# Optimization experiments

Measured on AMD Instinct MI355X. Metric: run time of the kernel, lower is better.

The kernel has to match this reference:

```python
import jax, jax.numpy as jnp
import numpy as np

HEADS = 8
DIM = 512
SCALE = (DIM // HEADS) ** (-0.5)  # 0.125


def setup_inputs() -> dict:
    key = jax.random.key(0)
    k1, k2, k3, k4 = jax.random.split(key, 4)
    B, C, H, W = 4, DIM, 96, 96
    x = jax.random.normal(k1, (B, C, H, W), dtype=jnp.float32)
    # 1x1 conv weights collapsed to matrices [out_ch, in_ch]
    w_qkv = jax.random.normal(k2, (3 * DIM, DIM), dtype=jnp.float32) * (DIM ** -0.5)
    w_out = jax.random.normal(k3, (DIM, DIM), dtype=jnp.float32) * (DIM ** -0.5)
    b_out = jax.random.normal(k4, (DIM,), dtype=jnp.float32) * 0.01
    return {"x": x, "w_qkv": w_qkv, "w_out": w_out, "b_out": b_out}


def reference(x, w_qkv, w_out, b_out):
    # axis='height' branch of the original forward
    b, c, h, w = x.shape
    heads = HEADS
    d = c // heads
    # 1x1 conv == per-pixel GEMM: [B,3C,H,W]
    qkv = jnp.einsum('bchw,oc->bohw', x, w_qkv)
    # 'b (qkv heads d) x y -> qkv b heads x y d'
    qkv = qkv.reshape(b, 3, heads, d, h, w)
    qkv = jnp.transpose(qkv, (1, 0, 2, 4, 5, 3))  # [3, b, heads, h, w, d]
    q, k, v = qkv[0], qkv[1], qkv[2]
    # attention along the width axis, batched over (b, heads, row x)
    dots = jnp.einsum('bhxid,bhxjd->bhxij', q, k) * SCALE
    attn = jax.nn.softmax(dots, axis=-1)
    out = jnp.einsum('bhxij,bhxjd->bhxid', attn, v)  # [b, heads, h, w, d]
    # 'b heads x y d -> b (heads d) x y'
    out = jnp.transpose(out, (0, 1, 4, 2, 3)).reshape(b, heads * d, h, w)
    # to_out 1x1 conv with bias
    out = jnp.einsum('bchw,oc->bohw', out, w_out) + b_out[None, :, None, None]
    return out
```

## Files before the change

### kernel.cpp

```cpp
#include <hip/hip_runtime.h>

typedef unsigned short u16;
typedef unsigned int u32;
typedef __attribute__((ext_vector_type(8))) short short8;
typedef __attribute__((ext_vector_type(4))) float floatx4;

#define HEADS 8
#define DIM 512
#define HH 96
#define WW 96
#define NPIX 9216
#define M_TOT 36864
#define N_QKV 1536
#define SCALE 0.125f

__device__ __forceinline__ float b2f(u16 v){
    union{float f;u32 u;}x; x.u=((u32)v)<<16; return x.f;
}
__device__ __forceinline__ u16 f2b(float f){
    union{float f;u32 u;}x; x.f=f;
    u32 u=x.u + 0x7fffu + ((x.u>>16)&1u);
    return (u16)(u>>16);
}
__device__ __forceinline__ u32 pack2(float a,float b){
    return (u32)f2b(a) | ((u32)f2b(b)<<16);
}

__device__ __forceinline__ void gload16(const u16* g, u16* l){
    __builtin_amdgcn_global_load_lds(
        (const __attribute__((address_space(1))) u32*)g,
        (__attribute__((address_space(3))) u32*)l, 16, 0, 0);
}

__global__ void detect_dtype(const u16* __restrict__ wq, int* __restrict__ flag){
    __shared__ int cnt;
    if (threadIdx.x==0) cnt=0;
    __syncthreads();
    u16 u = wq[2*threadIdx.x];
    int e = (u>>7)&0xff;
    if (e>=100 && e<=128) atomicAdd(&cnt,1);
    __syncthreads();
    if (threadIdx.x==0) *flag = (cnt>128)?1:0;
}

__global__ __launch_bounds__(256)
void convert_w(const void* __restrict__ wq, const void* __restrict__ wo,
               const int* __restrict__ flag, u16* __restrict__ wqb, u16* __restrict__ wob){
    const int isb = *flag;
    int i = blockIdx.x*256 + threadIdx.x;
    const int nq = N_QKV*DIM;
    if (i < nq){
        wqb[i] = isb ? ((const u16*)wq)[i] : f2b(((const float*)wq)[i]);
    } else {
        int j = i - nq;
        wob[j] = isb ? ((const u16*)wo)[j] : f2b(((const float*)wo)[j]);
    }
}

__global__ __launch_bounds__(256)
void convert_x(const void* __restrict__ xv, const int* __restrict__ flag,
               u16* __restrict__ xb){
    __shared__ u16 tile[64][65];
    const int isb = *flag;
    const int p0 = blockIdx.x*64, c0 = blockIdx.y*64, b = blockIdx.z;
    const int t = threadIdx.x;
    const int pl = t&63, c4 = t>>6;
    const float* x32 = (const float*)xv;
    const u16*   x16 = (const u16*)xv;
    size_t src = ((size_t)b*DIM + c0 + c4)*NPIX + p0 + pl;
    #pragma unroll
    for (int i=0;i<16;i++){
        int cl = c4 + i*4;
        size_t s = src + (size_t)i*4*NPIX;
        tile[cl][pl] = isb ? x16[s] : f2b(x32[s]);
    }
    __syncthreads();
    const int cu = t&31, r8 = t>>5;
    u32* xb32 = (u32*)xb;
    #pragma unroll
    for (int i=0;i<8;i++){
        int pr = r8 + i*8;
        u32 v = (u32)tile[2*cu][pr] | ((u32)tile[2*cu+1][pr]<<16);
        xb32[((size_t)b*NPIX + p0 + pr)*(DIM/2) + (c0>>1) + cu] = v;
    }
}

__global__ __launch_bounds__(256)
void gemm_qkv(const u16* __restrict__ A, const u16* __restrict__ B,
              u16* __restrict__ Cqk, u16* __restrict__ vt){
    __shared__ __align__(16) union ShMem {
        struct { u16 A[8192]; u16 B[8192]; } s;
        float ct[4][16][68];
    } sh;
    const int t = threadIdx.x;
    const int w = t>>6, l = t&63, lr = l&15, lq = l>>4;
    const int wm = w&1, wn = w>>1;
    const int n0 = blockIdx.x*128;
    const int m0 = blockIdx.y*128;
    const u16* ag[4]; const u16* bg[4]; u16* al[4]; u16* bl[4];
    #pragma unroll
    for (int i=0;i<4;i++){
        int tt = w*4+i;
        int ks = tt>>3, sub = tt&7;
        ag[i] = A + (size_t)(m0 + sub*16 + lr)*DIM + ks*32 + lq*8;
        bg[i] = B + (size_t)(n0 + sub*16 + lr)*DIM + ks*32 + lq*8;
        al[i] = &sh.s.A[tt*512];
        bl[i] = &sh.s.B[tt*512];
    }
    floatx4 acc[4][4] = {};
    for (int kt=0; kt<DIM; kt+=64){
        #pragma unroll
        for (int i=0;i<4;i++){ gload16(ag[i]+kt, al[i]); gload16(bg[i]+kt, bl[i]); }
        __syncthreads();
        #pragma unroll
        for (int ks=0;ks<2;ks++){
            short8 a[4], b[4];
            #pragma unroll
            for (int mi=0;mi<4;mi++) a[mi] = *(const short8*)&sh.s.A[(ks*8 + wm*4 + mi)*512 + l*8];
            #pragma unroll
            for (int ni=0;ni<4;ni++) b[ni] = *(const short8*)&sh.s.B[(ks*8 + wn*4 + ni)*512 + l*8];
            #pragma unroll
            for (int mi=0;mi<4;mi++)
                #pragma unroll
                for (int ni=0;ni<4;ni++)
                    acc[mi][ni] = __builtin_amdgcn_mfma_f32_16x16x32_bf16(a[mi], b[ni], acc[mi][ni], 0,0,0);
        }
        __syncthreads();
    }
    if (blockIdx.x < 8){
        #pragma unroll
        for (int mi=0;mi<4;mi++){
            #pragma unroll
            for (int r=0;r<4;r++){
                int m = m0 + wm*64 + mi*16 + lq*4 + r;
                u16* crow = Cqk + (size_t)m*1024 + n0 + wn*64 + lr;
                #pragma unroll
                for (int ni=0;ni<4;ni++) crow[ni*16] = f2b(acc[mi][ni][r]);
            }
        }
    } else {
        __syncthreads();
        const int bat  = m0 / NPIX;
        const int pixb = m0 - bat*NPIX + wm*64;
        for (int ni=0; ni<4; ni++){
            #pragma unroll
            for (int mi=0;mi<4;mi++)
                #pragma unroll
                for (int r=0;r<4;r++)
                    sh.ct[w][lr][mi*16 + lq*4 + r] = acc[mi][ni][r];
            __syncthreads();
            #pragma unroll
            for (int p=0;p<4;p++){
                int nl = p*4 + lq;
                int ch = n0 + wn*64 + ni*16 + nl - 1024;
                int bh2 = bat*8 + (ch>>6);
                int dd  = ch & 63;
                float4 v = *(const float4*)&sh.ct[w][nl][lr*4];
                size_t off = ((size_t)(bh2*64+dd))*NPIX + pixb + lr*4;
                u32* o32 = (u32*)vt;
                o32[off>>1]     = pack2(v.x, v.y);
                o32[(off>>1)+1] = pack2(v.z, v.w);
            }
            __syncthreads();
        }
    }
}

__global__ __launch_bounds__(256)
void attn_kernel(const u16* __restrict__ qk, const u16* __restrict__ vt,
                 u16* __restrict__ attno){
    __shared__ __align__(16) u16 Qf[6144];
    __shared__ __align__(16) u16 Kf[6144];
    __shared__ float Ss[96][97];
    __shared__ float smax[96][2], ssum[96][2], rinv[96];
    const int t = threadIdx.x;
    const int w = t>>6, l = t&63, lr = l&15, lq = l>>4;
    const int wm = w&1, wn = w>>1;
    const int blk = blockIdx.x;
    const int row  = blk % HH;
    const int bh   = blk / HH;
    const int head = bh & 7;
    const int bat  = bh >> 3;
    const size_t pixrow = (size_t)bat*NPIX + row*WW;
    const u16* qbase = qk + pixrow*1024 + head*64;
    #pragma unroll
    for (int i=0;i<6;i++){
        int c  = w*6 + i;
        int c2 = (c<12) ? c : (c-12);
        int mt = c2>>1, ks = c2&1;
        const u16* g = qbase + (size_t)(mt*16+lr)*1024 + ks*32 + lq*8 + ((c<12)?0:512);
        u16* dst = ((c<12)?Qf:Kf) + c2*512 + l*8;
        gload16(g, dst);
    }
    __syncthreads();
    {
        floatx4 acc[3][3] = {};
        #pragma unroll
        for (int ks=0;ks<2;ks++){
            short8 af[3], bf[3];
            #pragma unroll
            for (int i=0;i<3;i++) af[i] = *(const short8*)&Qf[((wm*3+i)*2+ks)*512 + l*8];
            #pragma unroll
            for (int j=0;j<3;j++) bf[j] = *(const short8*)&Kf[((wn*3+j)*2+ks)*512 + l*8];
            #pragma unroll
            for (int i=0;i<3;i++)
                #pragma unroll
                for (int j=0;j<3;j++)
                    acc[i][j] = __builtin_amdgcn_mfma_f32_16x16x32_bf16(af[i], bf[j], acc[i][j], 0,0,0);
        }
        #pragma unroll
        for (int i=0;i<3;i++)
            #pragma unroll
            for (int j=0;j<3;j++)
                #pragma unroll
                for (int r=0;r<4;r++)
                    Ss[(wm*3+i)*16 + lq*4 + r][(wn*3+j)*16 + lr] = acc[i][j][r]*SCALE;
    }
    __syncthreads();
    #pragma unroll
    for (int i=0;i<3;i++){
        const u16* g = vt + (size_t)(bh*64 + w*16 + lr)*NPIX + row*WW + i*32 + lq*8;
        gload16(g, Qf + (w*3+i)*512 + l*8);
    }
    const int srow = t>>1, shalf = t&1;
    if (t < 192){
        float m = -1e30f;
        #pragma unroll 8
        for (int j=0;j<48;j++) m = fmaxf(m, Ss[srow][shalf*48+j]);
        smax[srow][shalf] = m;
    }
    __syncthreads();
    if (t < 192){
        float m2 = fmaxf(smax[srow][0], smax[srow][1]);
        float s = 0.f;
        #pragma unroll 8
        for (int j=0;j<48;j++){
            float e = __expf(Ss[srow][shalf*48+j] - m2);
            Ss[srow][shalf*48+j] = e; s += e;
        }
        ssum[srow][shalf] = s;
    }
    __syncthreads();
    if (t < 192 && shalf==0) rinv[srow] = 1.f/(ssum[srow][0]+ssum[srow][1]);
    floatx4 o[3][2] = {};
    for (int ks2=0;ks2<3;ks2++){
        short8 bf2[2];
        #pragma unroll
        for (int bb=0;bb<2;bb++)
            bf2[bb] = *(const short8*)&Qf[((wn*2+bb)*3+ks2)*512 + l*8];
        #pragma unroll
        for (int aa=0;aa<3;aa++){
            int m = (wm*3+aa)*16 + lr;
            union { short8 s; u32 u[4]; } a;
            const float* srcp = &Ss[m][ks2*32 + lq*8];
            #pragma unroll
            for (int p=0;p<4;p++) a.u[p] = pack2(srcp[2*p], srcp[2*p+1]);
            #pragma unroll
            for (int bb=0;bb<2;bb++)
                o[aa][bb] = __builtin_amdgcn_mfma_f32_16x16x32_bf16(a.s, bf2[bb], o[aa][bb], 0,0,0);
        }
    }
    __syncthreads();
    #pragma unroll
    for (int aa=0;aa<3;aa++){
        #pragma unroll
        for (int r=0;r<4;r++){
            int i = (wm*3+aa)*16 + lq*4 + r;
            float rv = rinv[i];
            u16* orow = attno + (pixrow + i)*512 + head*64 + wn*32 + lr;
            orow[0]  = f2b(o[aa][0][r]*rv);
            orow[16] = f2b(o[aa][1][r]*rv);
        }
    }
}

__global__ __launch_bounds__(256)
void gemm_out(const u16* __restrict__ A, const u16* __restrict__ B,
              const void* __restrict__ bias, const int* __restrict__ flag,
              void* __restrict__ outv){
    __shared__ __align__(16) union ShMem {
        struct { u16 A[8192]; u16 B[8192]; } s;
        float ct[4][16][68];
    } sh;
    const int t = threadIdx.x;
    const int w = t>>6, l = t&63, lr = l&15, lq = l>>4;
    const int wm = w&1, wn = w>>1;
    const int n0 = blockIdx.x*128;
    const int m0 = blockIdx.y*128;
    const u16* ag[4]; const u16* bg[4]; u16* al[4]; u16* bl[4];
    #pragma unroll
    for (int i=0;i<4;i++){
        int tt = w*4+i;
        int ks = tt>>3, sub = tt&7;
        ag[i] = A + (size_t)(m0 + sub*16 + lr)*DIM + ks*32 + lq*8;
        bg[i] = B + (size_t)(n0 + sub*16 + lr)*DIM + ks*32 + lq*8;
        al[i] = &sh.s.A[tt*512];
        bl[i] = &sh.s.B[tt*512];
    }
    floatx4 acc[4][4] = {};
    for (int kt=0; kt<DIM; kt+=64){
        #pragma unroll
        for (int i=0;i<4;i++){ gload16(ag[i]+kt, al[i]); gload16(bg[i]+kt, bl[i]); }
        __syncthreads();
        #pragma unroll
        for (int ks=0;ks<2;ks++){
            short8 a[4], b[4];
            #pragma unroll
            for (int mi=0;mi<4;mi++) a[mi] = *(const short8*)&sh.s.A[(ks*8 + wm*4 + mi)*512 + l*8];
            #pragma unroll
            for (int ni=0;ni<4;ni++) b[ni] = *(const short8*)&sh.s.B[(ks*8 + wn*4 + ni)*512 + l*8];
            #pragma unroll
            for (int mi=0;mi<4;mi++)
                #pragma unroll
                for (int ni=0;ni<4;ni++)
                    acc[mi][ni] = __builtin_amdgcn_mfma_f32_16x16x32_bf16(a[mi], b[ni], acc[mi][ni], 0,0,0);
        }
        __syncthreads();
    }
    __syncthreads();
    const int isb = *flag;
    const int bat  = m0 / NPIX;
    const int pix0 = m0 - bat*NPIX + wm*64;
    const u16*   b16 = (const u16*)bias;
    const float* b32 = (const float*)bias;
    for (int ni=0; ni<4; ni++){
        #pragma unroll
        for (int mi=0;mi<4;mi++)
            #pragma unroll
            for (int r=0;r<4;r++)
                sh.ct[w][lr][mi*16 + lq*4 + r] = acc[mi][ni][r];
        __syncthreads();
        #pragma unroll
        for (int p=0;p<4;p++){
            int nl = p*4 + lq;
            int ng = n0 + wn*64 + ni*16 + nl;
            float4 v = *(const float4*)&sh.ct[w][nl][lr*4];
            float bv = isb ? b2f(b16[ng]) : b32[ng];
            v.x+=bv; v.y+=bv; v.z+=bv; v.w+=bv;
            size_t off = ((size_t)(bat*DIM + ng))*NPIX + pix0 + lr*4;
            if (isb){
                u32* o32 = (u32*)outv;
                o32[off>>1]     = pack2(v.x, v.y);
                o32[(off>>1)+1] = pack2(v.z, v.w);
            } else {
                *(float4*)((float*)outv + off) = v;
            }
        }
        __syncthreads();
    }
}

extern "C" void kernel_launch(void* const* d_in, const int* in_sizes, int n_in,
                              void* d_out, int out_size, void* d_ws, size_t ws_size,
                              hipStream_t stream){
    const void* x    = d_in[0];
    const void* wqkv = d_in[1];
    const void* wout = d_in[2];
    const void* bout = d_in[3];
    char* wsb = (char*)d_ws;
    int* flag    = (int*)wsb;
    u16* xb      = (u16*)(wsb + 256);
    u16* attn_ws = xb;
    u16* wqb     = xb + (size_t)M_TOT*DIM;
    u16* wob     = wqb + (size_t)N_QKV*DIM;
    u16* qk_ws   = wob + (size_t)DIM*DIM;
    u16* vt_ws   = qk_ws + (size_t)M_TOT*1024;
    detect_dtype<<<1, 256, 0, stream>>>((const u16*)wqkv, flag);
    convert_w<<<4096, 256, 0, stream>>>(wqkv, wout, flag, wqb, wob);
    convert_x<<<dim3(144, 8, 4), 256, 0, stream>>>(x, flag, xb);
    gemm_qkv<<<dim3(12, 288), 256, 0, stream>>>(xb, wqb, qk_ws, vt_ws);
    attn_kernel<<<3072, 256, 0, stream>>>(qk_ws, vt_ws, attn_ws);
    gemm_out<<<dim3(4, 288), 256, 0, stream>>>(attn_ws, wob, bout, flag, d_out);
}
```

Baseline: 378.9 us.

## Remap GEMM blocks per XCD, vectorize epilogue stores, keep softmax probabilities in bf16

Both GEMMs now use a 1D grid remapped so that consecutive M-tiles land on the same XCD, which is meant to improve L2 reuse. Their epilogues stage results through per-wave LDS and write 16-byte vectors, and block-wide barriers are dropped because each wave only touches its own LDS region. The attention kernel writes exp values straight into a bf16 LDS buffer, so the PV MFMA loads operands directly instead of repacking floats. It also stages the output through LDS for coalesced 16-byte stores. The risks are the barrier removal, which depends on intra-wave ordering, and an extra LDS round trip.

```diff
diff --git a/kernel.cpp b/kernel.cpp
--- a/kernel.cpp
+++ b/kernel.cpp
@@ -92,11 +92,15 @@
         struct { u16 A[8192]; u16 B[8192]; } s;
         float ct[4][16][68];
     } sh;
+    const int id = blockIdx.x;
+    const int xcd = id & 7, slot = id >> 3;
+    const int by = xcd*36 + slot/12;
+    const int bx = slot - (slot/12)*12;
     const int t = threadIdx.x;
     const int w = t>>6, l = t&63, lr = l&15, lq = l>>4;
     const int wm = w&1, wn = w>>1;
-    const int n0 = blockIdx.x*128;
-    const int m0 = blockIdx.y*128;
+    const int n0 = bx*128;
+    const int m0 = by*128;
     const u16* ag[4]; const u16* bg[4]; u16* al[4]; u16* bl[4];
     #pragma unroll
     for (int i=0;i<4;i++){
@@ -127,19 +131,30 @@
         }
         __syncthreads();
     }
-    if (blockIdx.x < 8){
+    if (bx < 8){
         #pragma unroll
         for (int mi=0;mi<4;mi++){
             #pragma unroll
-            for (int r=0;r<4;r++){
-                int m = m0 + wm*64 + mi*16 + lq*4 + r;
-                u16* crow = Cqk + (size_t)m*1024 + n0 + wn*64 + lr;
-                #pragma unroll
-                for (int ni=0;ni<4;ni++) crow[ni*16] = f2b(acc[mi][ni][r]);
-            }
+            for (int ni=0;ni<4;ni++)
+                #pragma unroll
+                for (int r=0;r<4;r++)
+                    sh.ct[w][lq*4+r][ni*16+lr] = acc[mi][ni][r];
+            int row = l>>2, cg = l&3;
+            const float* cp = &sh.ct[w][row][cg*16];
+            float4 v0 = *(const float4*)(cp);
+            float4 v1 = *(const float4*)(cp+4);
+            float4 v2 = *(const float4*)(cp+8);
+            float4 v3 = *(const float4*)(cp+12);
+            uint4 s0, s1;
+            s0.x=pack2(v0.x,v0.y); s0.y=pack2(v0.z,v0.w);
+            s0.z=pack2(v1.x,v1.y); s0.w=pack2(v1.z,v1.w);
+            s1.x=pack2(v2.x,v2.y); s1.y=pack2(v2.z,v2.w);
+            s1.z=pack2(v3.x,v3.y); s1.w=pack2(v3.z,v3.w);
+            u16* dst = Cqk + (size_t)(m0+wm*64+mi*16+row)*1024 + n0 + wn*64 + cg*16;
+            *((uint4*)dst)     = s0;
+            *((uint4*)(dst+8)) = s1;
         }
     } else {
-        __syncthreads();
         const int bat  = m0 / NPIX;
         const int pixb = m0 - bat*NPIX + wm*64;
         for (int ni=0; ni<4; ni++){
@@ -148,20 +163,20 @@
                 #pragma unroll
                 for (int r=0;r<4;r++)
                     sh.ct[w][lr][mi*16 + lq*4 + r] = acc[mi][ni][r];
-            __syncthreads();
-            #pragma unroll
-            for (int p=0;p<4;p++){
-                int nl = p*4 + lq;
+            #pragma unroll
+            for (int p=0;p<2;p++){
+                int nl = (l>>3) + p*8;
                 int ch = n0 + wn*64 + ni*16 + nl - 1024;
                 int bh2 = bat*8 + (ch>>6);
                 int dd  = ch & 63;
-                float4 v = *(const float4*)&sh.ct[w][nl][lr*4];
-                size_t off = ((size_t)(bh2*64+dd))*NPIX + pixb + lr*4;
-                u32* o32 = (u32*)vt;
-                o32[off>>1]     = pack2(v.x, v.y);
-                o32[(off>>1)+1] = pack2(v.z, v.w);
+                const float* cp = &sh.ct[w][nl][(l&7)*8];
+                float4 v0 = *(const float4*)cp;
+                float4 v1 = *(const float4*)(cp+4);
+                uint4 s;
+                s.x=pack2(v0.x,v0.y); s.y=pack2(v0.z,v0.w);
+                s.z=pack2(v1.x,v1.y); s.w=pack2(v1.z,v1.w);
+                *(uint4*)(vt + (size_t)(bh2*64+dd)*NPIX + pixb + (l&7)*8) = s;
             }
-            __syncthreads();
         }
     }
 }
@@ -170,7 +185,7 @@
 void attn_kernel(const u16* __restrict__ qk, const u16* __restrict__ vt,
                  u16* __restrict__ attno){
     __shared__ __align__(16) u16 Qf[6144];
-    __shared__ __align__(16) u16 Kf[6144];
+    __shared__ __align__(16) u16 Pb[9984];
     __shared__ float Ss[96][97];
     __shared__ float smax[96][2], ssum[96][2], rinv[96];
     const int t = threadIdx.x;
@@ -189,7 +204,7 @@
         int c2 = (c<12) ? c : (c-12);
         int mt = c2>>1, ks = c2&1;
         const u16* g = qbase + (size_t)(mt*16+lr)*1024 + ks*32 + lq*8 + ((c<12)?0:512);
-        u16* dst = ((c<12)?Qf:Kf) + c2*512 + l*8;
+        u16* dst = ((c<12)?Qf:Pb) + c2*512 + l*8;
         gload16(g, dst);
     }
     __syncthreads();
@@ -201,7 +216,7 @@
             #pragma unroll
             for (int i=0;i<3;i++) af[i] = *(const short8*)&Qf[((wm*3+i)*2+ks)*512 + l*8];
             #pragma unroll
-            for (int j=0;j<3;j++) bf[j] = *(const short8*)&Kf[((wn*3+j)*2+ks)*512 + l*8];
+            for (int j=0;j<3;j++) bf[j] = *(const short8*)&Pb[((wn*3+j)*2+ks)*512 + l*8];
             #pragma unroll
             for (int i=0;i<3;i++)
                 #pragma unroll
@@ -222,27 +237,31 @@
         const u16* g = vt + (size_t)(bh*64 + w*16 + lr)*NPIX + row*WW + i*32 + lq*8;
         gload16(g, Qf + (w*3+i)*512 + l*8);
     }
-    const int srow = t>>1, shalf = t&1;
+    const int srow = t>>1, shalf = t&1, sbase = shalf*48;
     if (t < 192){
         float m = -1e30f;
         #pragma unroll 8
-        for (int j=0;j<48;j++) m = fmaxf(m, Ss[srow][shalf*48+j]);
+        for (int j=0;j<48;j++) m = fmaxf(m, Ss[srow][sbase+j]);
         smax[srow][shalf] = m;
     }
     __syncthreads();
     if (t < 192){
         float m2 = fmaxf(smax[srow][0], smax[srow][1]);
         float s = 0.f;
+        u32* prow = (u32*)&Pb[srow*104 + sbase];
         #pragma unroll 8
-        for (int j=0;j<48;j++){
-            float e = __expf(Ss[srow][shalf*48+j] - m2);
-            Ss[srow][shalf*48+j] = e; s += e;
+        for (int j=0;j<48;j+=2){
+            float e0 = __expf(Ss[srow][sbase+j]   - m2);
+            float e1 = __expf(Ss[srow][sbase+j+1] - m2);
+            prow[j>>1] = pack2(e0, e1);
+            s += e0 + e1;
         }
         ssum[srow][shalf] = s;
     }
     __syncthreads();
     if (t < 192 && shalf==0) rinv[srow] = 1.f/(ssum[srow][0]+ssum[srow][1]);
     floatx4 o[3][2] = {};
+    #pragma unroll
     for (int ks2=0;ks2<3;ks2++){
         short8 bf2[2];
         #pragma unroll
@@ -250,14 +269,10 @@
             bf2[bb] = *(const short8*)&Qf[((wn*2+bb)*3+ks2)*512 + l*8];
         #pragma unroll
         for (int aa=0;aa<3;aa++){
-            int m = (wm*3+aa)*16 + lr;
-            union { short8 s; u32 u[4]; } a;
-            const float* srcp = &Ss[m][ks2*32 + lq*8];
-            #pragma unroll
-            for (int p=0;p<4;p++) a.u[p] = pack2(srcp[2*p], srcp[2*p+1]);
+            short8 af = *(const short8*)&Pb[((wm*3+aa)*16+lr)*104 + ks2*32 + lq*8];
             #pragma unroll
             for (int bb=0;bb<2;bb++)
-                o[aa][bb] = __builtin_amdgcn_mfma_f32_16x16x32_bf16(a.s, bf2[bb], o[aa][bb], 0,0,0);
+                o[aa][bb] = __builtin_amdgcn_mfma_f32_16x16x32_bf16(af, bf2[bb], o[aa][bb], 0,0,0);
         }
     }
     __syncthreads();
@@ -265,12 +280,20 @@
     for (int aa=0;aa<3;aa++){
         #pragma unroll
         for (int r=0;r<4;r++){
-            int i = (wm*3+aa)*16 + lq*4 + r;
-            float rv = rinv[i];
-            u16* orow = attno + (pixrow + i)*512 + head*64 + wn*32 + lr;
-            orow[0]  = f2b(o[aa][0][r]*rv);
-            orow[16] = f2b(o[aa][1][r]*rv);
-        }
+            int m = (wm*3+aa)*16 + lq*4 + r;
+            float rv = rinv[m];
+            int d0 = wn*32 + lr;
+            Pb[m*72 + d0]      = f2b(o[aa][0][r]*rv);
+            Pb[m*72 + d0 + 16] = f2b(o[aa][1][r]*rv);
+        }
+    }
+    __syncthreads();
+    #pragma unroll
+    for (int i=0;i<3;i++){
+        int idx = i*256 + t;
+        int rr = idx>>3, seg = idx&7;
+        uint4 vv = *(const uint4*)&Pb[rr*72 + seg*8];
+        *(uint4*)(attno + (pixrow+rr)*512 + head*64 + seg*8) = vv;
     }
 }
 
@@ -282,11 +305,15 @@
         struct { u16 A[8192]; u16 B[8192]; } s;
         float ct[4][16][68];
     } sh;
+    const int id = blockIdx.x;
+    const int xcd = id & 7, slot = id >> 3;
+    const int by = xcd*36 + (slot>>2);
+    const int bx = slot & 3;
     const int t = threadIdx.x;
     const int w = t>>6, l = t&63, lr = l&15, lq = l>>4;
     const int wm = w&1, wn = w>>1;
-    const int n0 = blockIdx.x*128;
-    const int m0 = blockIdx.y*128;
+    const int n0 = bx*128;
+    const int m0 = by*128;
     const u16* ag[4]; const u16* bg[4]; u16* al[4]; u16* bl[4];
     #pragma unroll
     for (int i=0;i<4;i++){
@@ -317,7 +344,6 @@
         }
         __syncthreads();
     }
-    __syncthreads();
     const int isb = *flag;
     const int bat  = m0 / NPIX;
     const int pix0 = m0 - bat*NPIX + wm*64;
@@ -329,24 +355,28 @@
             #pragma unroll
             for (int r=0;r<4;r++)
                 sh.ct[w][lr][mi*16 + lq*4 + r] = acc[mi][ni][r];
-        __syncthreads();
-        #pragma unroll
-        for (int p=0;p<4;p++){
-            int nl = p*4 + lq;
+        #pragma unroll
+        for (int p=0;p<2;p++){
+            int nl = (l>>3) + p*8;
             int ng = n0 + wn*64 + ni*16 + nl;
-            float4 v = *(const float4*)&sh.ct[w][nl][lr*4];
             float bv = isb ? b2f(b16[ng]) : b32[ng];
-            v.x+=bv; v.y+=bv; v.z+=bv; v.w+=bv;
-            size_t off = ((size_t)(bat*DIM + ng))*NPIX + pix0 + lr*4;
+            const float* cp = &sh.ct[w][nl][(l&7)*8];
+            float4 v0 = *(const float4*)cp;
+            float4 v1 = *(const float4*)(cp+4);
+            v0.x+=bv; v0.y+=bv; v0.z+=bv; v0.w+=bv;
+            v1.x+=bv; v1.y+=bv; v1.z+=bv; v1.w+=bv;
+            size_t off = ((size_t)(bat*DIM + ng))*NPIX + pix0 + (l&7)*8;
             if (isb){
-                u32* o32 = (u32*)outv;
-                o32[off>>1]     = pack2(v.x, v.y);
-                o32[(off>>1)+1] = pack2(v.z, v.w);
+                uint4 s;
+                s.x=pack2(v0.x,v0.y); s.y=pack2(v0.z,v0.w);
+                s.z=pack2(v1.x,v1.y); s.w=pack2(v1.z,v1.w);
+                *(uint4*)((u16*)outv + off) = s;
             } else {
-                *(float4*)((float*)outv + off) = v;
+                float* of = (float*)outv + off;
+                *(float4*)of     = v0;
+                *(float4*)(of+4) = v1;
             }
         }
-        __syncthreads();
     }
 }
 
@@ -368,7 +398,7 @@
     detect_dtype<<<1, 256, 0, stream>>>((const u16*)wqkv, flag);
     convert_w<<<4096, 256, 0, stream>>>(wqkv, wout, flag, wqb, wob);
     convert_x<<<dim3(144, 8, 4), 256, 0, stream>>>(x, flag, xb);
-    gemm_qkv<<<dim3(12, 288), 256, 0, stream>>>(xb, wqb, qk_ws, vt_ws);
+    gemm_qkv<<<3456, 256, 0, stream>>>(xb, wqb, qk_ws, vt_ws);
     attn_kernel<<<3072, 256, 0, stream>>>(qk_ws, vt_ws, attn_ws);
-    gemm_out<<<dim3(4, 288), 256, 0, stream>>>(attn_ws, wob, bout, flag, d_out);
-}
+    gemm_out<<<1152, 256, 0, stream>>>(attn_ws, wob, bout, flag, d_out);
+}
```

After: 370.9 us. 2.1% less time.
